# Kernel tuning notes

Hardware: AMD Instinct MI355X
Metric: run time of the kernel (lower is better)

The kernel has to match this reference:

```python
import jax, jax.numpy as jnp
import numpy as np
import math

EPS = 1e-5
GN_GROUPS = 32


def conv2d(x, w, padding):
    # x: [B,C,H,W], w: [O,I,kh,kw]
    return jax.lax.conv_general_dilated(
        x, w, window_strides=(1, 1), padding=[(padding, padding)] * 2,
        dimension_numbers=("NCHW", "OIHW", "NCHW"))


def group_norm(x, weight, bias, groups=GN_GROUPS, eps=EPS):
    B, C, H, W = x.shape
    xg = x.reshape(B, groups, C // groups, H, W)
    mu = xg.mean(axis=(2, 3, 4), keepdims=True)
    var = xg.var(axis=(2, 3, 4), keepdims=True)
    xn = (xg - mu) * jax.lax.rsqrt(var + eps)
    xn = xn.reshape(B, C, H, W)
    return xn * weight[None, :, None, None] + bias[None, :, None, None]


def setup_inputs() -> dict:
    key = jax.random.key(0)
    ks = jax.random.split(key, 8)
    B, C, H, W = 8, 256, 80, 80
    init_gate = 0.99
    gate_bias_val = 0.5 * math.log((1 + init_gate) / (1 - init_gate))
    return {
        "x": jax.random.normal(ks[0], (B, C, H, W), dtype=jnp.float32),
        "w1": jax.random.normal(ks[1], (C, C, 3, 3), dtype=jnp.float32) * 0.01,
        "gn1_w": jnp.ones((C,), dtype=jnp.float32),
        "gn1_b": jnp.zeros((C,), dtype=jnp.float32),
        "w2": jax.random.normal(ks[2], (C, C, 3, 3), dtype=jnp.float32) * 0.01,
        "gn2_w": jnp.ones((C,), dtype=jnp.float32),
        "gn2_b": jnp.zeros((C,), dtype=jnp.float32),
        "gate_w": jax.random.normal(ks[3], (1, C, 1, 1), dtype=jnp.float32) * 0.01,
        "gate_b": jnp.full((1,), gate_bias_val, dtype=jnp.float32),
    }


def reference(x, w1, gn1_w, gn1_b, w2, gn2_w, gn2_b, gate_w, gate_b):
    # shortcut is identity (in_channels == out_channels, stride 1)
    shortcut = x
    # conv1 -> GN -> ReLU
    h = jax.nn.relu(group_norm(conv2d(x, w1, padding=1), gn1_w, gn1_b))
    # conv2 -> GN
    h = group_norm(conv2d(h, w2, padding=1), gn2_w, gn2_b)
    # SpatialGate: 1x1 conv on the original input, ReTanH activation
    g = conv2d(x, gate_w, padding=0) + gate_b[None, :, None, None]  # [B,1,H,W]
    gate = jnp.clip(jnp.tanh(g), 0.0, None)
    # num_groups == 1: encode/decode are identity reshapes; gate broadcasts over C
    out = h * gate
    return jax.nn.relu(out + shortcut)
```

## Files before the change

kernel.cpp:

```cpp
#include <hip/hip_runtime.h>
#include <math.h>

#define NB   8
#define NC   256
#define NH   80
#define NW   80
#define NHW  6400
#define GN_EPS 1e-5f

typedef __bf16 bf16;
typedef bf16 bf16x2 __attribute__((ext_vector_type(2)));
typedef bf16 bf16x4 __attribute__((ext_vector_type(4)));
typedef bf16 bf16x8 __attribute__((ext_vector_type(8)));
typedef float f32x4 __attribute__((ext_vector_type(4)));

typedef __attribute__((address_space(1))) void gvoid;
typedef __attribute__((address_space(3))) void lvoid;
__device__ __forceinline__ void glds16(const void* g, void* l) {
    __builtin_amdgcn_global_load_lds((const gvoid*)g, (lvoid*)l, 16, 0, 0);
}

#define TT_Q 4616
#define AW_Q 520
#define AW_T 2080

__global__ __launch_bounds__(256) void setup_kernel(
    const float* __restrict__ w1, const float* __restrict__ w2,
    bf16* __restrict__ wA1, bf16* __restrict__ wA2,
    float* __restrict__ gacc, float* __restrict__ stats)
{
    int blk = blockIdx.x, tid = threadIdx.x;
    if (blk < 200) { gacc[blk * 256 + tid] = 0.0f; return; }
    if (blk == 200) {
        #pragma unroll
        for (int k = 0; k < 8; k++) stats[tid + k * 256] = 0.0f;
        return;
    }
    int rb = blk - 201;
    const float* w = (rb < 2304) ? w1 : w2;
    bf16* wA       = (rb < 2304) ? wA1 : wA2;
    int idx = (rb % 2304) * 256 + tid;
    int c8 = idx & 7;
    int co = (idx >> 3) & 255;
    int qq = (idx >> 11) & 3;
    int tc = idx >> 13;
    int tap = tc % 9, chunk = tc / 9;
    int ci = chunk * 32 + qq * 8 + c8;
    wA[idx] = (bf16)w[(size_t)(co * 256 + ci) * 9 + tap];
}

__global__ __launch_bounds__(256) void prep1_kernel(
    const float* __restrict__ x, bf16* __restrict__ xp,
    const float* __restrict__ gw, float* __restrict__ gacc)
{
    __shared__ float tile[8 * 84];
    int bid = blockIdx.x;
    int row = bid % 80;
    int cib = (bid / 80) & 31;
    int b   = bid / 2560;
    for (int e = threadIdx.x; e < 640; e += 256) {
        int c8 = e / 80, col = e - c8 * 80;
        tile[c8 * 84 + col] = x[((size_t)(b * NC + cib * 8 + c8) * NH + row) * NW + col];
    }
    __syncthreads();
    size_t base = (((size_t)(b * 32 + cib) * 82 + row + 1) * 82) * 8 + 8;
    for (int t = threadIdx.x; t < 320; t += 256) {
        int e = 2 * t, col = e >> 3, c8 = e & 7;
        bf16x2 pk = { (bf16)tile[c8 * 84 + col], (bf16)tile[(c8 + 1) * 84 + col] };
        *(bf16x2*)(xp + base + e) = pk;
    }
    if (threadIdx.x < 80) {
        int col = threadIdx.x;
        float s = 0.0f;
        #pragma unroll
        for (int c8 = 0; c8 < 8; c8++) s = fmaf(tile[c8 * 84 + col], gw[cib * 8 + c8], s);
        atomicAdd(gacc + (size_t)b * NHW + row * 80 + col, s);
    }
    const uint4 z4 = make_uint4(0u, 0u, 0u, 0u);
    size_t img = ((size_t)(b * 32 + cib)) * 82;
    if (threadIdx.x < 2) {
        int col = threadIdx.x * 81;
        *(uint4*)(xp + ((img + row + 1) * 82 + col) * 8) = z4;
    }
    if (row == 0 || row == 79) {
        int prow = (row == 0) ? 0 : 81;
        for (int u = threadIdx.x; u < 82; u += 256)
            *(uint4*)(xp + ((img + prow) * 82 + u) * 8) = z4;
    }
}

__global__ __launch_bounds__(256) void gate_fin_kernel(
    float* __restrict__ gacc, const float* __restrict__ gb)
{
    int i = blockIdx.x * 256 + threadIdx.x;
    gacc[i] = fmaxf(tanhf(gacc[i] + gb[0]), 0.0f);
}

__global__ __launch_bounds__(320, 3) void conv_kernel(
    const bf16* __restrict__ xp, const bf16* __restrict__ wA,
    bf16* __restrict__ y, float* __restrict__ ssum, float* __restrict__ ssq)
{
    __shared__ __align__(16) bf16 Tt[4 * TT_Q];
    __shared__ __align__(16) bf16 Aw[9 * AW_T];
    __shared__ float wgs[8], wgq[8];

    int tid  = threadIdx.x;
    int wid  = tid >> 6;
    int lane = tid & 63;
    int n = lane & 15, q = lane >> 4;

    int bid = blockIdx.x;
    int b   = bid >> 6;
    int rem = bid & 63;
    int ct  = rem >> 4;
    int rt  = rem & 15;
    int co0 = ct * 64, h0 = rt * 5;

    if (tid < 8) { wgs[tid] = 0.0f; wgq[tid] = 0.0f; }

    f32x4 acc[4][5];
    #pragma unroll
    for (int i = 0; i < 4; i++)
        #pragma unroll
        for (int j = 0; j < 5; j++) acc[i][j] = (f32x4){0.f, 0.f, 0.f, 0.f};

    for (int c = 0; c < 8; c++) {
        __syncthreads();
        if (wid < 4) {
            const char* s8 = (const char*)(xp +
                (((size_t)(b * 32 + c * 4 + wid) * 82 + h0) * 82) * 8);
            char* l8 = (char*)(Tt + wid * TT_Q);
            #pragma unroll
            for (int u = 0; u < 9; u++)
                glds16(s8 + u * 1024 + lane * 16, l8 + u * 1024);
        }
        for (int p = wid; p < 36; p += 5) {
            int tap = p >> 2, qq = p & 3;
            const char* s8 = (const char*)(wA + ((size_t)(c * 36 + p) * 256 + co0) * 8);
            char* l8 = (char*)(Aw + tap * AW_T + qq * AW_Q);
            glds16(s8 + lane * 16, l8);
        }
        __syncthreads();

        #pragma unroll
        for (int tap = 0; tap < 9; tap++) {
            const int r = tap / 3, s = tap - 3 * r;
            bf16x8 af[4], bfr[5];
            #pragma unroll
            for (int mt = 0; mt < 4; mt++)
                af[mt] = *(const bf16x8*)(Aw + tap * AW_T + q * AW_Q + (mt * 16 + n) * 8);
            #pragma unroll
            for (int nt = 0; nt < 5; nt++)
                bfr[nt] = *(const bf16x8*)(Tt + q * TT_Q + (wid + r) * 656 + (s + nt * 16 + n) * 8);
            #pragma unroll
            for (int mt = 0; mt < 4; mt++)
                #pragma unroll
                for (int nt = 0; nt < 5; nt++)
                    acc[mt][nt] = __builtin_amdgcn_mfma_f32_16x16x32_bf16(
                        af[mt], bfr[nt], acc[mt][nt], 0, 0, 0);
        }
    }

    int h = h0 + wid;
    #pragma unroll
    for (int mt = 0; mt < 4; mt++) {
        float s1 = 0.0f, s2 = 0.0f;
        int co  = co0 + mt * 16 + q * 4;
        int cib = co >> 3, c8 = co & 7;
        #pragma unroll
        for (int nt = 0; nt < 5; nt++) {
            int col = nt * 16 + n;
            bf16x4 pk;
            #pragma unroll
            for (int rg = 0; rg < 4; rg++) {
                float v = acc[mt][nt][rg];
                pk[rg] = (bf16)v;
                s1 += v;
                s2 = fmaf(v, v, s2);
            }
            *(bf16x4*)(y + ((((size_t)(b * 32 + cib) * 80 + h) * 80 + col) * 8 + c8)) = pk;
        }
        #pragma unroll
        for (int off = 1; off < 16; off <<= 1) {
            s1 += __shfl_xor(s1, off, 64);
            s2 += __shfl_xor(s2, off, 64);
        }
        if (n == 0) {
            int gl = mt * 2 + (q >> 1);
            atomicAdd(&wgs[gl], s1);
            atomicAdd(&wgq[gl], s2);
        }
    }
    __syncthreads();
    if (tid < 8) {
        atomicAdd(&ssum[b * 32 + ct * 8 + tid], wgs[tid]);
        atomicAdd(&ssq [b * 32 + ct * 8 + tid], wgq[tid]);
    }
}

__global__ void statfin_kernel(const float* __restrict__ s, const float* __restrict__ sq,
                               float* __restrict__ mu, float* __restrict__ rs)
{
    int i = threadIdx.x;
    const float cnt = (float)(8 * NHW);
    float m = s[i] / cnt;
    float v = sq[i] / cnt - m * m;
    mu[i] = m;
    rs[i] = rsqrtf(v + GN_EPS);
}

__global__ __launch_bounds__(256) void prep2_kernel(
    const bf16* __restrict__ y, bf16* __restrict__ xp,
    const float* __restrict__ mu, const float* __restrict__ rs,
    const float* __restrict__ gamma, const float* __restrict__ beta)
{
    int bid = blockIdx.x;
    int b = bid / 640; int rem = bid - b * 640;
    int cib = rem / 20; int rq = rem - cib * 20;
    int gidx = b * 32 + cib;
    float m = mu[gidx], r = rs[gidx];
    const bf16* src = y + (size_t)(b * 32 + cib) * 51200 + rq * 2560;
    for (int u = threadIdx.x; u < 1280; u += 256) {
        int e = 2 * u;
        int row = rq * 4 + e / 640;
        int w640 = e % 640;
        int c8 = e & 7;
        int c = cib * 8 + c8;
        float sc0 = r * gamma[c],     sh0 = beta[c]     - m * sc0;
        float sc1 = r * gamma[c + 1], sh1 = beta[c + 1] - m * sc1;
        bf16x2 iv = *(const bf16x2*)(src + e);
        bf16x2 pk = { (bf16)fmaxf(fmaf((float)iv[0], sc0, sh0), 0.0f),
                      (bf16)fmaxf(fmaf((float)iv[1], sc1, sh1), 0.0f) };
        size_t xidx = (((size_t)(b * 32 + cib) * 82 + row + 1) * 82) * 8 + 8 + w640;
        *(bf16x2*)(xp + xidx) = pk;
    }
}

__global__ __launch_bounds__(256) void final_kernel(
    const bf16* __restrict__ y, const float* __restrict__ x,
    const float* __restrict__ gate,
    const float* __restrict__ mu, const float* __restrict__ rs,
    const float* __restrict__ gamma, const float* __restrict__ beta,
    float* __restrict__ out)
{
    __shared__ float lds[8 * 324];
    int bid = blockIdx.x;
    int b = bid / 640; int rem = bid - b * 640;
    int cib = rem / 20; int rq = rem - cib * 20;
    int gidx = b * 32 + cib;
    float m = mu[gidx], r = rs[gidx];
    const bf16* src = y + (size_t)(b * 32 + cib) * 51200 + rq * 2560;
    for (int u = threadIdx.x; u < 1280; u += 256) {
        int e = 2 * u;
        int c8 = e & 7;
        int rc = e >> 3;
        int c = cib * 8 + c8;
        float sc0 = r * gamma[c],     sh0 = beta[c]     - m * sc0;
        float sc1 = r * gamma[c + 1], sh1 = beta[c + 1] - m * sc1;
        bf16x2 iv = *(const bf16x2*)(src + e);
        lds[c8 * 324 + rc]       = fmaf((float)iv[0], sc0, sh0);
        lds[(c8 + 1) * 324 + rc] = fmaf((float)iv[1], sc1, sh1);
    }
    __syncthreads();
    const float* gp = gate + b * NHW + rq * 320;
    for (int e2 = threadIdx.x; e2 < 2560; e2 += 256) {
        int c8 = e2 / 320, rc = e2 - c8 * 320;
        int c = cib * 8 + c8;
        size_t oidx = (size_t)(b * NC + c) * NHW + rq * 320 + rc;
        float v = fmaf(lds[c8 * 324 + rc], gp[rc], x[oidx]);
        out[oidx] = fmaxf(v, 0.0f);
    }
}

extern "C" void kernel_launch(void* const* d_in, const int* in_sizes, int n_in,
                              void* d_out, int out_size, void* d_ws, size_t ws_size,
                              hipStream_t stream)
{
    const float* x     = (const float*)d_in[0];
    const float* w1    = (const float*)d_in[1];
    const float* gn1_w = (const float*)d_in[2];
    const float* gn1_b = (const float*)d_in[3];
    const float* w2    = (const float*)d_in[4];
    const float* gn2_w = (const float*)d_in[5];
    const float* gn2_b = (const float*)d_in[6];
    const float* gw    = (const float*)d_in[7];
    const float* gb    = (const float*)d_in[8];

    bf16*  xp  = (bf16*)d_out;
    float* out = (float*)d_out;

    char* wsb = (char*)d_ws;
    bf16*  y     = (bf16*)wsb;
    float* gacc  = (float*)(wsb + 26214400);
    bf16*  wA1   = (bf16*)(wsb + 26214400 + 204800);
    bf16*  wA2   = wA1 + 589824;
    float* stats = (float*)(wsb + 26214400 + 204800 + 2 * 1179648);
    float* s1  = stats,        * s1q = stats + 256;
    float* mu1 = stats + 512,  * rs1 = stats + 768;
    float* s2  = stats + 1024, * s2q = stats + 1280;
    float* mu2 = stats + 1536, * rs2 = stats + 1792;

    setup_kernel<<<4809, 256, 0, stream>>>(w1, w2, wA1, wA2, gacc, stats);
    prep1_kernel<<<20480, 256, 0, stream>>>(x, xp, gw, gacc);
    gate_fin_kernel<<<200, 256, 0, stream>>>(gacc, gb);
    conv_kernel<<<512, 320, 0, stream>>>(xp, wA1, y, s1, s1q);
    statfin_kernel<<<1, 256, 0, stream>>>(s1, s1q, mu1, rs1);
    prep2_kernel<<<5120, 256, 0, stream>>>(y, xp, mu1, rs1, gn1_w, gn1_b);
    conv_kernel<<<512, 320, 0, stream>>>(xp, wA2, y, s2, s2q);
    statfin_kernel<<<1, 256, 0, stream>>>(s2, s2q, mu2, rs2);
    final_kernel<<<5120, 256, 0, stream>>>(y, x, gacc, mu2, rs2, gn2_w, gn2_b, out);
}
```

Measured before the change: 320.3 us.

## Read conv activations from global, double-buffer weights in LDS, drop gate atomics

The conv kernel no longer stages the padded activation tile in LDS. Each lane loads its B fragments straight from global memory, and the weight chunks are double-buffered in LDS so the load for chunk c+1 is issued while chunk c is computed, with one barrier per iteration instead of two. The gate 1x1 conv now writes per-channel-block partial sums into spare output memory, and gate_fin reduces them, which removes the float atomics and the gacc zeroing. The cost is repeated, overlapping global or cache reads for the 9 taps directly in the MFMA loop, plus reliance on the barrier to order the asynchronous LDS loads.

New measurement: 329.9 us. 1.03x slower.

```diff
diff --git a/kernel.cpp b/kernel.cpp
--- a/kernel.cpp
+++ b/kernel.cpp
@@ -20,23 +20,22 @@
     __builtin_amdgcn_global_load_lds((const gvoid*)g, (lvoid*)l, 16, 0, 0);
 }
 
-#define TT_Q 4616
 #define AW_Q 520
 #define AW_T 2080
+#define AW_BUF 18720
 
 __global__ __launch_bounds__(256) void setup_kernel(
     const float* __restrict__ w1, const float* __restrict__ w2,
     bf16* __restrict__ wA1, bf16* __restrict__ wA2,
-    float* __restrict__ gacc, float* __restrict__ stats)
+    float* __restrict__ stats)
 {
     int blk = blockIdx.x, tid = threadIdx.x;
-    if (blk < 200) { gacc[blk * 256 + tid] = 0.0f; return; }
-    if (blk == 200) {
+    if (blk == 0) {
         #pragma unroll
         for (int k = 0; k < 8; k++) stats[tid + k * 256] = 0.0f;
         return;
     }
-    int rb = blk - 201;
+    int rb = blk - 1;
     const float* w = (rb < 2304) ? w1 : w2;
     bf16* wA       = (rb < 2304) ? wA1 : wA2;
     int idx = (rb % 2304) * 256 + tid;
@@ -51,7 +50,7 @@
 
 __global__ __launch_bounds__(256) void prep1_kernel(
     const float* __restrict__ x, bf16* __restrict__ xp,
-    const float* __restrict__ gw, float* __restrict__ gacc)
+    const float* __restrict__ gw, float* __restrict__ gpart)
 {
     __shared__ float tile[8 * 84];
     int bid = blockIdx.x;
@@ -74,7 +73,7 @@
         float s = 0.0f;
         #pragma unroll
         for (int c8 = 0; c8 < 8; c8++) s = fmaf(tile[c8 * 84 + col], gw[cib * 8 + c8], s);
-        atomicAdd(gacc + (size_t)b * NHW + row * 80 + col, s);
+        gpart[((size_t)cib * NB + b) * NHW + row * 80 + col] = s;
     }
     const uint4 z4 = make_uint4(0u, 0u, 0u, 0u);
     size_t img = ((size_t)(b * 32 + cib)) * 82;
@@ -90,18 +89,21 @@
 }
 
 __global__ __launch_bounds__(256) void gate_fin_kernel(
-    float* __restrict__ gacc, const float* __restrict__ gb)
+    const float* __restrict__ gpart, const float* __restrict__ gb,
+    float* __restrict__ gate)
 {
     int i = blockIdx.x * 256 + threadIdx.x;
-    gacc[i] = fmaxf(tanhf(gacc[i] + gb[0]), 0.0f);
+    float s = gb[0];
+    #pragma unroll 8
+    for (int k = 0; k < 32; k++) s += gpart[(size_t)k * (NB * NHW) + i];
+    gate[i] = fmaxf(tanhf(s), 0.0f);
 }
 
 __global__ __launch_bounds__(320, 3) void conv_kernel(
     const bf16* __restrict__ xp, const bf16* __restrict__ wA,
     bf16* __restrict__ y, float* __restrict__ ssum, float* __restrict__ ssq)
 {
-    __shared__ __align__(16) bf16 Tt[4 * TT_Q];
-    __shared__ __align__(16) bf16 Aw[9 * AW_T];
+    __shared__ __align__(16) bf16 Aw[2 * AW_BUF];
     __shared__ float wgs[8], wgq[8];
 
     int tid  = threadIdx.x;
@@ -124,23 +126,24 @@
         #pragma unroll
         for (int j = 0; j < 5; j++) acc[i][j] = (f32x4){0.f, 0.f, 0.f, 0.f};
 
+    for (int p = wid; p < 36; p += 5) {
+        int tap = p >> 2, qq = p & 3;
+        glds16((const char*)(wA + ((size_t)(0 * 36 + p) * 256 + co0) * 8) + lane * 16,
+               (char*)(Aw + tap * AW_T + qq * AW_Q) + lane * 16);
+    }
+
     for (int c = 0; c < 8; c++) {
         __syncthreads();
-        if (wid < 4) {
-            const char* s8 = (const char*)(xp +
-                (((size_t)(b * 32 + c * 4 + wid) * 82 + h0) * 82) * 8);
-            char* l8 = (char*)(Tt + wid * TT_Q);
-            #pragma unroll
-            for (int u = 0; u < 9; u++)
-                glds16(s8 + u * 1024 + lane * 16, l8 + u * 1024);
-        }
-        for (int p = wid; p < 36; p += 5) {
-            int tap = p >> 2, qq = p & 3;
-            const char* s8 = (const char*)(wA + ((size_t)(c * 36 + p) * 256 + co0) * 8);
-            char* l8 = (char*)(Aw + tap * AW_T + qq * AW_Q);
-            glds16(s8 + lane * 16, l8);
-        }
-        __syncthreads();
+        if (c + 1 < 8) {
+            bf16* dst = Aw + (((c + 1) & 1) ? AW_BUF : 0);
+            for (int p = wid; p < 36; p += 5) {
+                int tap = p >> 2, qq = p & 3;
+                glds16((const char*)(wA + ((size_t)((c + 1) * 36 + p) * 256 + co0) * 8) + lane * 16,
+                       (char*)(dst + tap * AW_T + qq * AW_Q) + lane * 16);
+            }
+        }
+        const bf16* awc = Aw + ((c & 1) ? AW_BUF : 0) + q * AW_Q + n * 8;
+        const bf16* xq = xp + (((size_t)(b * 32 + c * 4 + q) * 82 + (h0 + wid)) * 82) * 8 + n * 8;
 
         #pragma unroll
         for (int tap = 0; tap < 9; tap++) {
@@ -148,10 +151,10 @@
             bf16x8 af[4], bfr[5];
             #pragma unroll
             for (int mt = 0; mt < 4; mt++)
-                af[mt] = *(const bf16x8*)(Aw + tap * AW_T + q * AW_Q + (mt * 16 + n) * 8);
+                af[mt] = *(const bf16x8*)(awc + tap * AW_T + mt * 128);
             #pragma unroll
             for (int nt = 0; nt < 5; nt++)
-                bfr[nt] = *(const bf16x8*)(Tt + q * TT_Q + (wid + r) * 656 + (s + nt * 16 + n) * 8);
+                bfr[nt] = *(const bf16x8*)(xq + (r * 82 + s + nt * 16) * 8);
             #pragma unroll
             for (int mt = 0; mt < 4; mt++)
                 #pragma unroll
@@ -286,12 +289,13 @@
     const float* gw    = (const float*)d_in[7];
     const float* gb    = (const float*)d_in[8];
 
-    bf16*  xp  = (bf16*)d_out;
-    float* out = (float*)d_out;
+    bf16*  xp    = (bf16*)d_out;
+    float* gpart = (float*)((char*)d_out + 27541504);
+    float* out   = (float*)d_out;
 
     char* wsb = (char*)d_ws;
     bf16*  y     = (bf16*)wsb;
-    float* gacc  = (float*)(wsb + 26214400);
+    float* gate  = (float*)(wsb + 26214400);
     bf16*  wA1   = (bf16*)(wsb + 26214400 + 204800);
     bf16*  wA2   = wA1 + 589824;
     float* stats = (float*)(wsb + 26214400 + 204800 + 2 * 1179648);
@@ -300,13 +304,13 @@
     float* s2  = stats + 1024, * s2q = stats + 1280;
     float* mu2 = stats + 1536, * rs2 = stats + 1792;
 
-    setup_kernel<<<4809, 256, 0, stream>>>(w1, w2, wA1, wA2, gacc, stats);
-    prep1_kernel<<<20480, 256, 0, stream>>>(x, xp, gw, gacc);
-    gate_fin_kernel<<<200, 256, 0, stream>>>(gacc, gb);
+    setup_kernel<<<4609, 256, 0, stream>>>(w1, w2, wA1, wA2, stats);
+    prep1_kernel<<<20480, 256, 0, stream>>>(x, xp, gw, gpart);
+    gate_fin_kernel<<<200, 256, 0, stream>>>(gpart, gb, gate);
     conv_kernel<<<512, 320, 0, stream>>>(xp, wA1, y, s1, s1q);
     statfin_kernel<<<1, 256, 0, stream>>>(s1, s1q, mu1, rs1);
     prep2_kernel<<<5120, 256, 0, stream>>>(y, xp, mu1, rs1, gn1_w, gn1_b);
     conv_kernel<<<512, 320, 0, stream>>>(xp, wA2, y, s2, s2q);
     statfin_kernel<<<1, 256, 0, stream>>>(s2, s2q, mu2, rs2);
-    final_kernel<<<5120, 256, 0, stream>>>(y, x, gacc, mu2, rs2, gn2_w, gn2_b, out);
-}
+    final_kernel<<<5120, 256, 0, stream>>>(y, x, gate, mu2, rs2, gn2_w, gn2_b, out);
+}
```
